# Optimization experiments

Measured on AMD Instinct MI355X. Metric: run time of the kernel, lower is better.

Reference implementation:

```python
import jax, jax.numpy as jnp
import numpy as np

B, T, F, UNITS = 64, 512, 128, 512
EPS = 1e-3  # Keras LayerNormalization default epsilon


def _layer_norm(x, g, b):
    m = x.mean(-1, keepdims=True)
    v = x.var(-1, keepdims=True)
    return (x - m) * jax.lax.rsqrt(v + EPS) * g + b


def _lstm(x, W, U, b):
    # Keras LSTM, gate order [i, f, c, o], zero initial state, tanh activations.
    Bsz = x.shape[0]
    Un = U.shape[0]
    h0 = jnp.zeros((Bsz, Un), x.dtype)
    c0 = jnp.zeros((Bsz, Un), x.dtype)
    xW = x @ W + b  # precompute input projection: [B, T, 4U]

    def step(carry, xw_t):
        h, c = carry
        z = xw_t + h @ U
        i, f, g, o = jnp.split(z, 4, axis=-1)
        c = jax.nn.sigmoid(f) * c + jax.nn.sigmoid(i) * jnp.tanh(g)
        h = jax.nn.sigmoid(o) * jnp.tanh(c)
        return (h, c), h

    (h, c), hs = jax.lax.scan(step, (h0, c0), jnp.swapaxes(xW, 0, 1))
    return jnp.swapaxes(hs, 0, 1), h, c  # seq out [B,T,U], final h, c


def _block(x, l0, l1, Wt, bt):
    block_in = x
    # layer 0: LSTM -> LayerNorm
    W, U, b, g, be = l0
    h, _, _ = _lstm(x, W, U, b)
    out = _layer_norm(h, g, be)
    # layer 1: LSTM -> LayerNorm -> Highway (units match layer 0)
    W, U, b, g, be = l1
    h, _, _ = _lstm(out, W, U, b)
    Hx = _layer_norm(h, g, be)
    Tx = jax.nn.sigmoid(out @ Wt + bt)  # transform gate, bias init -1.5
    hw = Hx * Tx + (1.0 - Tx) * out
    # quasi-dense: concat block input with last layer output
    return jnp.concatenate([block_in, hw], axis=-1)


def setup_inputs() -> dict:
    key = jax.random.key(0)
    ks = iter(jax.random.split(key, 32))
    def nrm(shape, scale):
        return jax.random.normal(next(ks), shape, jnp.float32) * scale
    d = {"x": jax.random.normal(next(ks), (B, T, F), jnp.float32)}
    in_dims = {"00": F, "01": UNITS, "10": F + UNITS, "11": UNITS}
    for tag, ind in in_dims.items():
        d[f"W{tag}"] = nrm((ind, 4 * UNITS), 1.0 / np.sqrt(ind))
        d[f"U{tag}"] = nrm((UNITS, 4 * UNITS), 1.0 / np.sqrt(UNITS))
        d[f"b{tag}"] = jnp.zeros((4 * UNITS,), jnp.float32)
        d[f"g{tag}"] = jnp.ones((UNITS,), jnp.float32)
        d[f"be{tag}"] = jnp.zeros((UNITS,), jnp.float32)
    for blk in ("0", "1"):
        d[f"Wt{blk}"] = nrm((UNITS, UNITS), 1.0 / np.sqrt(UNITS))
        d[f"bt{blk}"] = jnp.full((UNITS,), -1.5, jnp.float32)
    return d


def reference(x,
              W00, U00, b00, g00, be00,
              W01, U01, b01, g01, be01,
              Wt0, bt0,
              W10, U10, b10, g10, be10,
              W11, U11, b11, g11, be11,
              Wt1, bt1):
    out0 = _block(x, (W00, U00, b00, g00, be00), (W01, U01, b01, g01, be01), Wt0, bt0)
    out1 = _block(out0, (W10, U10, b10, g10, be10), (W11, U11, b11, g11, be11), Wt1, bt1)
    return out1  # [B, T, F + 2*UNITS]
```

## Files before the change

### kernel.cpp

```cpp
#include <hip/hip_runtime.h>
#include <hip/hip_bf16.h>

typedef unsigned short u16;
typedef unsigned int u32;
typedef __attribute__((ext_vector_type(8))) short short8;
typedef __attribute__((ext_vector_type(4))) short short4v;
typedef __attribute__((ext_vector_type(4))) float float4v;

#define Bsz 64
#define Tsz 512
#define Fsz 128
#define Usz 512
#define Gsz 2048
#define Msz 32768
#define OUTW 1152
#define BINW 640
#define NWG 16

__device__ __forceinline__ u16 f2b(float f) {
  u32 u = __float_as_uint(f);
  u32 r = (u + 0x7fffu + ((u >> 16) & 1u)) >> 16;
  return (u16)r;
}
__device__ __forceinline__ float b2f(u16 h) {
  return __uint_as_float(((u32)h) << 16);
}
__device__ __forceinline__ float sigm(float x) { return 1.f / (1.f + __expf(-x)); }
__device__ __forceinline__ float tanhfast(float x) { return 2.f / (1.f + __expf(-2.f * x)) - 1.f; }

__global__ void k_wt(const float* __restrict__ src, u16* __restrict__ dst, int K, int N) {
  __shared__ float t[32][33];
  int k0 = blockIdx.y << 5, n0 = blockIdx.x << 5;
  int tid = threadIdx.x;
  int r = tid >> 3, c = (tid & 7) << 2;
  float4v v = *(const float4v*)(src + (size_t)(k0 + r) * N + n0 + c);
  t[r][c + 0] = v[0]; t[r][c + 1] = v[1]; t[r][c + 2] = v[2]; t[r][c + 3] = v[3];
  __syncthreads();
  short4v o;
  o[0] = (short)f2b(t[c + 0][r]);
  o[1] = (short)f2b(t[c + 1][r]);
  o[2] = (short)f2b(t[c + 2][r]);
  o[3] = (short)f2b(t[c + 3][r]);
  *(short4v*)(dst + (size_t)(n0 + r) * K + k0 + c) = o;
}

__global__ void k_cvx(const float* __restrict__ x, float* __restrict__ dout, u16* __restrict__ bin) {
  int id = blockIdx.x * 256 + threadIdx.x;
  int row = id >> 5, c = (id & 31) << 2;
  float4v v = *(const float4v*)(x + (size_t)row * Fsz + c);
  *(float4v*)(dout + (size_t)row * OUTW + c) = v;
  short4v o;
  o[0] = (short)f2b(v[0]); o[1] = (short)f2b(v[1]);
  o[2] = (short)f2b(v[2]); o[3] = (short)f2b(v[3]);
  *(short4v*)(bin + (size_t)row * BINW + c) = o;
}

template <int PERM>
__launch_bounds__(256)
__global__ void k_gemm(const u16* __restrict__ A, int lda,
                       const u16* __restrict__ Bt, int K, int N,
                       const float* __restrict__ bias,
                       u16* __restrict__ C) {
  __shared__ u16 Al[128][40];
  __shared__ u16 Bl[64][40];
  int tid = threadIdx.x;
  int lane = tid & 63, wid = tid >> 6;
  int n0 = blockIdx.x << 6;
  size_t m0 = (size_t)blockIdx.y << 7;
  int mr = lane & 15, ko = (lane >> 4) << 3;
  float4v acc[2][4];
#pragma unroll
  for (int i = 0; i < 2; ++i)
#pragma unroll
    for (int j = 0; j < 4; ++j) acc[i][j] = (float4v){0.f, 0.f, 0.f, 0.f};

  for (int k0 = 0; k0 < K; k0 += 32) {
#pragma unroll
    for (int i = 0; i < 2; ++i) {
      int id = tid + (i << 8);
      int row = id >> 2, kc = (id & 3) << 3;
      int mlog = (int)m0 + row;
      size_t rp = PERM ? ((size_t)(mlog & 63) << 9) + (mlog >> 6) : (size_t)mlog;
      *(short8*)&Al[row][kc] = *(const short8*)(A + rp * (size_t)lda + k0 + kc);
    }
    {
      int row = tid >> 2, kc = (tid & 3) << 3;
      *(short8*)&Bl[row][kc] = *(const short8*)(Bt + (size_t)(n0 + row) * K + k0 + kc);
    }
    __syncthreads();
    short8 af0 = *(short8*)&Al[(wid << 5) + mr][ko];
    short8 af1 = *(short8*)&Al[(wid << 5) + 16 + mr][ko];
    short8 bf0 = *(short8*)&Bl[mr][ko];
    short8 bf1 = *(short8*)&Bl[16 + mr][ko];
    short8 bf2 = *(short8*)&Bl[32 + mr][ko];
    short8 bf3 = *(short8*)&Bl[48 + mr][ko];
    acc[0][0] = __builtin_amdgcn_mfma_f32_16x16x32_bf16(af0, bf0, acc[0][0], 0, 0, 0);
    acc[0][1] = __builtin_amdgcn_mfma_f32_16x16x32_bf16(af0, bf1, acc[0][1], 0, 0, 0);
    acc[0][2] = __builtin_amdgcn_mfma_f32_16x16x32_bf16(af0, bf2, acc[0][2], 0, 0, 0);
    acc[0][3] = __builtin_amdgcn_mfma_f32_16x16x32_bf16(af0, bf3, acc[0][3], 0, 0, 0);
    acc[1][0] = __builtin_amdgcn_mfma_f32_16x16x32_bf16(af1, bf0, acc[1][0], 0, 0, 0);
    acc[1][1] = __builtin_amdgcn_mfma_f32_16x16x32_bf16(af1, bf1, acc[1][1], 0, 0, 0);
    acc[1][2] = __builtin_amdgcn_mfma_f32_16x16x32_bf16(af1, bf2, acc[1][2], 0, 0, 0);
    acc[1][3] = __builtin_amdgcn_mfma_f32_16x16x32_bf16(af1, bf3, acc[1][3], 0, 0, 0);
    __syncthreads();
  }
  int rbase = (lane >> 4) << 2;
#pragma unroll
  for (int mt = 0; mt < 2; ++mt)
#pragma unroll
    for (int nt = 0; nt < 4; ++nt) {
      int n = n0 + (nt << 4) + mr;
      float bv = bias[n];
#pragma unroll
      for (int r = 0; r < 4; ++r) {
        int mlog = (int)m0 + (wid << 5) + (mt << 4) + rbase + r;
        float val = acc[mt][nt][r] + bv;
        if (PERM) {
          int b = mlog & 63, tt = mlog >> 6;
          int u = n & 511, g = n >> 9;
          C[(((size_t)tt * 512 + u) * 4 + g) * 64 + b] = f2b(val);
        } else {
          C[(size_t)mlog * N + n] = f2b(val);
        }
      }
    }
}

__global__ void k_zero(u32* __restrict__ p, int n32) {
  int id = blockIdx.x * 256 + threadIdx.x;
  for (int i = id; i < n32; i += gridDim.x * 256) p[i] = 0u;
}

__launch_bounds__(256, 1)
__global__ void k_scan(const u16* __restrict__ xw2,
                       const u16* __restrict__ Ut,
                       u16* __restrict__ hn,
                       u16* __restrict__ hseq,
                       u32* __restrict__ bar) {
  __shared__ u16 hl[32768];
  int tid = threadIdx.x;
  int lane = tid & 63, wid = tid >> 6;
  int mr = lane & 15, cg = lane >> 4;
  int ko = cg << 3;
  int gate = mr & 3, du = mr >> 2;
  int u0 = (blockIdx.x << 5) + (wid << 3);

  short8 af[2][16];
#pragma unroll
  for (int mt = 0; mt < 2; ++mt) {
    size_t urow = (size_t)(gate * Usz + u0 + (mt << 2) + du) * Usz;
#pragma unroll
    for (int kk = 0; kk < 16; ++kk)
      af[mt][kk] = *(const short8*)(Ut + urow + (kk << 5) + ko);
  }

  float cst[2][4];
#pragma unroll
  for (int mt = 0; mt < 2; ++mt)
#pragma unroll
    for (int nt = 0; nt < 4; ++nt) cst[mt][nt] = 0.f;

  u16 xwv[2][4][4], xwn[2][4][4];
#pragma unroll
  for (int mt = 0; mt < 2; ++mt) {
    int u = u0 + (mt << 2) + cg;
#pragma unroll
    for (int g = 0; g < 4; ++g)
#pragma unroll
      for (int nt = 0; nt < 4; ++nt)
        xwv[mt][g][nt] = xw2[(((size_t)0 * 512 + u) * 4 + g) * 64 + (nt << 4) + mr];
  }

  for (int t = 0; t < Tsz; ++t) {
    const u16* hsrc = hn + ((t & 1) ? 32768 : 0);
    u16* hdst = hn + ((t & 1) ? 0 : 32768);

    {
      const char* src = (const char*)hsrc;
#pragma unroll
      for (int j = 0; j < 16; ++j) {
        int b = (wid << 4) + j;
        int soff = ((lane << 4) ^ ((b & 7) << 4));
        __builtin_amdgcn_global_load_lds(
            (const __attribute__((address_space(1))) void*)(src + (size_t)b * 1024 + soff),
            (__attribute__((address_space(3))) void*)((char*)hl + (b << 10)),
            16, 0, 0);
      }
    }

    if (t + 1 < Tsz) {
#pragma unroll
      for (int mt = 0; mt < 2; ++mt) {
        int u = u0 + (mt << 2) + cg;
#pragma unroll
        for (int g = 0; g < 4; ++g)
#pragma unroll
          for (int nt = 0; nt < 4; ++nt)
            xwn[mt][g][nt] = xw2[(((size_t)(t + 1) * 512 + u) * 4 + g) * 64 + (nt << 4) + mr];
      }
    }

    float4v acc[2][4];
#pragma unroll
    for (int mt = 0; mt < 2; ++mt)
#pragma unroll
      for (int nt = 0; nt < 4; ++nt)
        acc[mt][nt] = (float4v){b2f(xwv[mt][0][nt]), b2f(xwv[mt][1][nt]),
                                b2f(xwv[mt][2][nt]), b2f(xwv[mt][3][nt])};

    __syncthreads();

#pragma unroll
    for (int kk = 0; kk < 16; ++kk) {
      short8 bfr[4];
#pragma unroll
      for (int nt = 0; nt < 4; ++nt) {
        int b = (nt << 4) + mr;
        int addr = (b << 10) + ((((kk << 6) + (cg << 4)) ^ ((b & 7) << 4)));
        bfr[nt] = *(const short8*)((const char*)hl + addr);
      }
#pragma unroll
      for (int mt = 0; mt < 2; ++mt)
#pragma unroll
        for (int nt = 0; nt < 4; ++nt)
          acc[mt][nt] = __builtin_amdgcn_mfma_f32_16x16x32_bf16(af[mt][kk], bfr[nt], acc[mt][nt], 0, 0, 0);
    }

#pragma unroll
    for (int mt = 0; mt < 2; ++mt)
#pragma unroll
      for (int nt = 0; nt < 4; ++nt) {
        float zi = acc[mt][nt][0], zf = acc[mt][nt][1];
        float zg = acc[mt][nt][2], zo = acc[mt][nt][3];
        float c = sigm(zf) * cst[mt][nt] + sigm(zi) * tanhfast(zg);
        cst[mt][nt] = c;
        float h = sigm(zo) * tanhfast(c);
        u16 hb = f2b(h);
        int b = (nt << 4) + mr;
        int u = u0 + (mt << 2) + cg;
        hdst[(size_t)b * Usz + u] = hb;
        hseq[((size_t)b * Tsz + t) * Usz + u] = hb;
      }

    if (t + 1 < Tsz) {
#pragma unroll
      for (int mt = 0; mt < 2; ++mt)
#pragma unroll
        for (int g = 0; g < 4; ++g)
#pragma unroll
          for (int nt = 0; nt < 4; ++nt) xwv[mt][g][nt] = xwn[mt][g][nt];
    }

    __syncthreads();
    if (tid == 0) {
      __threadfence();
      __hip_atomic_fetch_add(bar, 1u, __ATOMIC_RELEASE, __HIP_MEMORY_SCOPE_AGENT);
      u32 target = (u32)NWG * (u32)(t + 1);
      while (__hip_atomic_load(bar, __ATOMIC_ACQUIRE, __HIP_MEMORY_SCOPE_AGENT) < target)
        __builtin_amdgcn_s_sleep(1);
      __threadfence();
    }
    __syncthreads();
  }
}

__launch_bounds__(256)
__global__ void k_ln(const u16* __restrict__ in, const float* __restrict__ g,
                     const float* __restrict__ be, u16* __restrict__ out) {
  int lane = threadIdx.x & 63, wid = threadIdx.x >> 6;
  size_t row = (size_t)blockIdx.x * 4 + wid;
  short8 v = *(const short8*)(in + row * Usz + (lane << 3));
  float f[8];
  float s = 0.f, q = 0.f;
#pragma unroll
  for (int j = 0; j < 8; ++j) { f[j] = b2f((u16)v[j]); s += f[j]; q += f[j] * f[j]; }
#pragma unroll
  for (int o = 32; o > 0; o >>= 1) { s += __shfl_xor(s, o); q += __shfl_xor(q, o); }
  float mean = s * (1.f / 512.f);
  float var = q * (1.f / 512.f) - mean * mean;
  float rs = rsqrtf(var + 1e-3f);
  float4v g0 = *(const float4v*)(g + (lane << 3));
  float4v g1 = *(const float4v*)(g + (lane << 3) + 4);
  float4v e0 = *(const float4v*)(be + (lane << 3));
  float4v e1 = *(const float4v*)(be + (lane << 3) + 4);
  short8 o8;
#pragma unroll
  for (int j = 0; j < 8; ++j) {
    float gg = (j < 4) ? g0[j] : g1[j - 4];
    float ee = (j < 4) ? e0[j] : e1[j - 4];
    o8[j] = (short)f2b((f[j] - mean) * rs * gg + ee);
  }
  *(short8*)(out + row * Usz + (lane << 3)) = o8;
}

__launch_bounds__(256)
__global__ void k_lnhw(const u16* __restrict__ hs, const float* __restrict__ g,
                       const float* __restrict__ be, const u16* __restrict__ txr,
                       const u16* __restrict__ ob, float* __restrict__ dout,
                       int dcol, u16* __restrict__ bin) {
  int lane = threadIdx.x & 63, wid = threadIdx.x >> 6;
  size_t row = (size_t)blockIdx.x * 4 + wid;
  short8 v = *(const short8*)(hs + row * Usz + (lane << 3));
  float f[8];
  float s = 0.f, q = 0.f;
#pragma unroll
  for (int j = 0; j < 8; ++j) { f[j] = b2f((u16)v[j]); s += f[j]; q += f[j] * f[j]; }
#pragma unroll
  for (int o = 32; o > 0; o >>= 1) { s += __shfl_xor(s, o); q += __shfl_xor(q, o); }
  float mean = s * (1.f / 512.f);
  float var = q * (1.f / 512.f) - mean * mean;
  float rs = rsqrtf(var + 1e-3f);
  float4v g0 = *(const float4v*)(g + (lane << 3));
  float4v g1 = *(const float4v*)(g + (lane << 3) + 4);
  float4v e0 = *(const float4v*)(be + (lane << 3));
  float4v e1 = *(const float4v*)(be + (lane << 3) + 4);
  short8 tv = *(const short8*)(txr + row * Usz + (lane << 3));
  short8 ov = *(const short8*)(ob + row * Usz + (lane << 3));
  float hwv[8];
#pragma unroll
  for (int j = 0; j < 8; ++j) {
    float gg = (j < 4) ? g0[j] : g1[j - 4];
    float ee = (j < 4) ? e0[j] : e1[j - 4];
    float hx = (f[j] - mean) * rs * gg + ee;
    float tx = sigm(b2f((u16)tv[j]));
    float o_ = b2f((u16)ov[j]);
    hwv[j] = hx * tx + (1.f - tx) * o_;
  }
  float4v w0 = {hwv[0], hwv[1], hwv[2], hwv[3]};
  float4v w1 = {hwv[4], hwv[5], hwv[6], hwv[7]};
  *(float4v*)(dout + row * OUTW + dcol + (lane << 3)) = w0;
  *(float4v*)(dout + row * OUTW + dcol + (lane << 3) + 4) = w1;
  if (bin) {
    short8 hb;
#pragma unroll
    for (int j = 0; j < 8; ++j) hb[j] = (short)f2b(hwv[j]);
    *(short8*)(bin + row * BINW + 128 + (lane << 3)) = hb;
  }
}

extern "C" void kernel_launch(void* const* d_in, const int* in_sizes, int n_in,
                              void* d_out, int out_size, void* d_ws, size_t ws_size,
                              hipStream_t stream) {
  (void)in_sizes; (void)n_in; (void)out_size; (void)ws_size;
  const float* x = (const float*)d_in[0];
  const float* W[4]  = {(const float*)d_in[1],  (const float*)d_in[6],
                        (const float*)d_in[11], (const float*)d_in[16]};
  const float* U[4]  = {(const float*)d_in[2],  (const float*)d_in[7],
                        (const float*)d_in[12], (const float*)d_in[17]};
  const float* bb_[4] = {(const float*)d_in[3],  (const float*)d_in[8],
                        (const float*)d_in[13], (const float*)d_in[18]};
  const float* gg_[4] = {(const float*)d_in[4],  (const float*)d_in[9],
                        (const float*)d_in[14], (const float*)d_in[19]};
  const float* be_[4] = {(const float*)d_in[5],  (const float*)d_in[10],
                        (const float*)d_in[15], (const float*)d_in[20]};
  const float* Wtr[2] = {(const float*)d_in[21], (const float*)d_in[23]};
  const float* btr[2] = {(const float*)d_in[22], (const float*)d_in[24]};

  char* ws = (char*)d_ws;
  size_t off = 0;
  u16* xwb  = (u16*)(ws + off); off += (size_t)Msz * Gsz * 2;
  u16* hseq = (u16*)(ws + off); off += (size_t)Msz * Usz * 2;
  u16* mid  = (u16*)(ws + off); off += (size_t)Msz * Usz * 2;
  u16* bin  = (u16*)(ws + off); off += (size_t)Msz * BINW * 2;
  const int KIN[4] = {128, 512, 640, 512};
  u16* Wtb[4];
  for (int i = 0; i < 4; ++i) { Wtb[i] = (u16*)(ws + off); off += (size_t)Gsz * KIN[i] * 2; }
  u16* Utb[4];
  for (int i = 0; i < 4; ++i) { Utb[i] = (u16*)(ws + off); off += (size_t)Gsz * Usz * 2; }
  u16* Wtrb[2];
  for (int i = 0; i < 2; ++i) { Wtrb[i] = (u16*)(ws + off); off += (size_t)Usz * Usz * 2; }
  u16* hn = (u16*)(ws + off); off += 2 * (size_t)Bsz * Usz * 2;
  u32* bar = (u32*)(ws + off); off += 256;
  float* dout = (float*)d_out;

  for (int i = 0; i < 4; ++i)
    k_wt<<<dim3(Gsz / 32, KIN[i] / 32), 256, 0, stream>>>(W[i], Wtb[i], KIN[i], Gsz);
  for (int i = 0; i < 4; ++i)
    k_wt<<<dim3(Gsz / 32, Usz / 32), 256, 0, stream>>>(U[i], Utb[i], Usz, Gsz);
  for (int i = 0; i < 2; ++i)
    k_wt<<<dim3(Usz / 32, Usz / 32), 256, 0, stream>>>(Wtr[i], Wtrb[i], Usz, Usz);

  k_cvx<<<(Msz * 32) / 256, 256, 0, stream>>>(x, dout, bin);

  for (int blk = 0; blk < 2; ++blk) {
    int l0 = blk * 2, l1 = blk * 2 + 1;
    k_gemm<1><<<dim3(Gsz / 64, Msz / 128), 256, 0, stream>>>(bin, BINW, Wtb[l0], KIN[l0], Gsz, bb_[l0], xwb);
    k_zero<<<32, 256, 0, stream>>>((u32*)hn, 32768 + 64);
    k_scan<<<NWG, 256, 0, stream>>>(xwb, Utb[l0], hn, hseq, bar);
    k_ln<<<Msz / 4, 256, 0, stream>>>(hseq, gg_[l0], be_[l0], mid);
    k_gemm<1><<<dim3(Gsz / 64, Msz / 128), 256, 0, stream>>>(mid, Usz, Wtb[l1], Usz, Gsz, bb_[l1], xwb);
    k_zero<<<32, 256, 0, stream>>>((u32*)hn, 32768 + 64);
    k_scan<<<NWG, 256, 0, stream>>>(xwb, Utb[l1], hn, hseq, bar);
    k_gemm<0><<<dim3(Usz / 64, Msz / 128), 256, 0, stream>>>(mid, Usz, Wtrb[blk], Usz, Usz, btr[blk], xwb);
    k_lnhw<<<Msz / 4, 256, 0, stream>>>(hseq, gg_[l1], be_[l1], xwb, mid, dout,
                                        blk == 0 ? 128 : 640, blk == 0 ? bin : (u16*)nullptr);
  }
}
```

Before: 13.09 ms.

## Replace atomic counter barrier with per-WG flags and read h from hseq directly

The scan kernel drops the double-buffered h scratch and reads the previous step's hidden state straight from a time-major hseq buffer. A single atomic counter barrier is replaced by per-workgroup padded flags polled by one wavefront. It also adds coalesced LDS-staged h writes, gate-interleaved xW loads as short4 vectors, and launches 128 blocks of which only every eighth works, presumably to spread the active workgroups across XCDs. Downstream the LN/GEMM stages are re-permuted to consume time-major hseq, which risks layout bugs but cuts barrier contention and scattered stores.

```diff
diff --git a/kernel.cpp b/kernel.cpp
--- a/kernel.cpp
+++ b/kernel.cpp
@@ -6,6 +6,8 @@
 typedef __attribute__((ext_vector_type(8))) short short8;
 typedef __attribute__((ext_vector_type(4))) short short4v;
 typedef __attribute__((ext_vector_type(4))) float float4v;
+typedef __attribute__((ext_vector_type(2))) unsigned int uint2v;
+typedef __attribute__((ext_vector_type(4))) unsigned int uint4v;
 
 #define Bsz 64
 #define Tsz 512
@@ -16,6 +18,7 @@
 #define OUTW 1152
 #define BINW 640
 #define NWG 16
+#define FLSTR 32
 
 __device__ __forceinline__ u16 f2b(float f) {
   u32 u = __float_as_uint(f);
@@ -55,7 +58,7 @@
   *(short4v*)(bin + (size_t)row * BINW + c) = o;
 }
 
-template <int PERM>
+template <int APERM, int CPERM>
 __launch_bounds__(256)
 __global__ void k_gemm(const u16* __restrict__ A, int lda,
                        const u16* __restrict__ Bt, int K, int N,
@@ -80,7 +83,7 @@
       int id = tid + (i << 8);
       int row = id >> 2, kc = (id & 3) << 3;
       int mlog = (int)m0 + row;
-      size_t rp = PERM ? ((size_t)(mlog & 63) << 9) + (mlog >> 6) : (size_t)mlog;
+      size_t rp = APERM ? ((size_t)(mlog & 63) << 9) + (mlog >> 6) : (size_t)mlog;
       *(short8*)&Al[row][kc] = *(const short8*)(A + rp * (size_t)lda + k0 + kc);
     }
     {
@@ -115,10 +118,10 @@
       for (int r = 0; r < 4; ++r) {
         int mlog = (int)m0 + (wid << 5) + (mt << 4) + rbase + r;
         float val = acc[mt][nt][r] + bv;
-        if (PERM) {
+        if (CPERM) {
           int b = mlog & 63, tt = mlog >> 6;
           int u = n & 511, g = n >> 9;
-          C[(((size_t)tt * 512 + u) * 4 + g) * 64 + b] = f2b(val);
+          C[((((size_t)tt * 512 + u) * 64 + b) << 2) + g] = f2b(val);
         } else {
           C[(size_t)mlog * N + n] = f2b(val);
         }
@@ -134,16 +137,17 @@
 __launch_bounds__(256, 1)
 __global__ void k_scan(const u16* __restrict__ xw2,
                        const u16* __restrict__ Ut,
-                       u16* __restrict__ hn,
                        u16* __restrict__ hseq,
                        u32* __restrict__ bar) {
+  if (blockIdx.x & 7) return;
+  int wg = blockIdx.x >> 3;
   __shared__ u16 hl[32768];
+  u16* hout = hl;
   int tid = threadIdx.x;
   int lane = tid & 63, wid = tid >> 6;
   int mr = lane & 15, cg = lane >> 4;
-  int ko = cg << 3;
   int gate = mr & 3, du = mr >> 2;
-  int u0 = (blockIdx.x << 5) + (wid << 3);
+  int u0 = (wg << 5) + (wid << 3);
 
   short8 af[2][16];
 #pragma unroll
@@ -151,7 +155,7 @@
     size_t urow = (size_t)(gate * Usz + u0 + (mt << 2) + du) * Usz;
 #pragma unroll
     for (int kk = 0; kk < 16; ++kk)
-      af[mt][kk] = *(const short8*)(Ut + urow + (kk << 5) + ko);
+      af[mt][kk] = *(const short8*)(Ut + urow + (kk << 5) + (cg << 3));
   }
 
   float cst[2][4];
@@ -160,72 +164,75 @@
 #pragma unroll
     for (int nt = 0; nt < 4; ++nt) cst[mt][nt] = 0.f;
 
-  u16 xwv[2][4][4], xwn[2][4][4];
-#pragma unroll
-  for (int mt = 0; mt < 2; ++mt) {
-    int u = u0 + (mt << 2) + cg;
-#pragma unroll
-    for (int g = 0; g < 4; ++g)
+  short4v xwc[2][4], xwn[2][4];
+#pragma unroll
+  for (int mt = 0; mt < 2; ++mt)
+#pragma unroll
+    for (int nt = 0; nt < 4; ++nt)
+      xwc[mt][nt] = *(const short4v*)(xw2 + ((((size_t)0 * 512 + u0 + (mt << 2) + cg) * 64
+                                             + (nt << 4) + mr) << 2));
+
+  for (int t = 0; t < Tsz; ++t) {
+    float4v acc[2][4];
+#pragma unroll
+    for (int mt = 0; mt < 2; ++mt)
 #pragma unroll
       for (int nt = 0; nt < 4; ++nt)
-        xwv[mt][g][nt] = xw2[(((size_t)0 * 512 + u) * 4 + g) * 64 + (nt << 4) + mr];
-  }
-
-  for (int t = 0; t < Tsz; ++t) {
-    const u16* hsrc = hn + ((t & 1) ? 32768 : 0);
-    u16* hdst = hn + ((t & 1) ? 0 : 32768);
-
-    {
-      const char* src = (const char*)hsrc;
-#pragma unroll
-      for (int j = 0; j < 16; ++j) {
-        int b = (wid << 4) + j;
-        int soff = ((lane << 4) ^ ((b & 7) << 4));
-        __builtin_amdgcn_global_load_lds(
-            (const __attribute__((address_space(1))) void*)(src + (size_t)b * 1024 + soff),
-            (__attribute__((address_space(3))) void*)((char*)hl + (b << 10)),
-            16, 0, 0);
-      }
-    }
+        acc[mt][nt] = (float4v){b2f((u16)xwc[mt][nt][0]), b2f((u16)xwc[mt][nt][1]),
+                                b2f((u16)xwc[mt][nt][2]), b2f((u16)xwc[mt][nt][3])};
 
     if (t + 1 < Tsz) {
 #pragma unroll
-      for (int mt = 0; mt < 2; ++mt) {
-        int u = u0 + (mt << 2) + cg;
-#pragma unroll
-        for (int g = 0; g < 4; ++g)
+      for (int mt = 0; mt < 2; ++mt)
+#pragma unroll
+        for (int nt = 0; nt < 4; ++nt)
+          xwn[mt][nt] = *(const short4v*)(xw2 + ((((size_t)(t + 1) * 512 + u0 + (mt << 2) + cg) * 64
+                                                 + (nt << 4) + mr) << 2));
+    }
+
+    if (t > 0) {
+      if (wid == 0) {
+        u32 tgt = (u32)t;
+        for (;;) {
+          u32 v = (lane < NWG)
+                    ? __hip_atomic_load(bar + lane * FLSTR, __ATOMIC_RELAXED, __HIP_MEMORY_SCOPE_AGENT)
+                    : 0xFFFFFFFFu;
+          if (__all(v >= tgt)) break;
+          __builtin_amdgcn_s_sleep(1);
+        }
+        __threadfence();
+      }
+      __syncthreads();
+
+      {
+        const char* hsrc = (const char*)hseq + ((size_t)(t - 1) << 16);
+#pragma unroll
+        for (int j = 0; j < 16; ++j) {
+          int c = (wid << 4) + j;
+          const char* src = hsrc + ((((c & 3) << 4) + mr) << 10) + ((c >> 2) << 6) + (cg << 4);
+          __builtin_amdgcn_global_load_lds(
+              (const __attribute__((address_space(1))) void*)src,
+              (__attribute__((address_space(3))) void*)(hl + (c << 9)),
+              16, 0, 0);
+        }
+      }
+      __syncthreads();
+
+#pragma unroll
+      for (int kk = 0; kk < 16; ++kk) {
+        short8 bfr[4];
+#pragma unroll
+        for (int nt = 0; nt < 4; ++nt)
+          bfr[nt] = *(const short8*)(hl + ((((kk << 2) + nt) << 9) + (lane << 3)));
+#pragma unroll
+        for (int mt = 0; mt < 2; ++mt)
 #pragma unroll
           for (int nt = 0; nt < 4; ++nt)
-            xwn[mt][g][nt] = xw2[(((size_t)(t + 1) * 512 + u) * 4 + g) * 64 + (nt << 4) + mr];
-      }
-    }
-
-    float4v acc[2][4];
-#pragma unroll
-    for (int mt = 0; mt < 2; ++mt)
-#pragma unroll
-      for (int nt = 0; nt < 4; ++nt)
-        acc[mt][nt] = (float4v){b2f(xwv[mt][0][nt]), b2f(xwv[mt][1][nt]),
-                                b2f(xwv[mt][2][nt]), b2f(xwv[mt][3][nt])};
-
-    __syncthreads();
-
-#pragma unroll
-    for (int kk = 0; kk < 16; ++kk) {
-      short8 bfr[4];
-#pragma unroll
-      for (int nt = 0; nt < 4; ++nt) {
-        int b = (nt << 4) + mr;
-        int addr = (b << 10) + ((((kk << 6) + (cg << 4)) ^ ((b & 7) << 4)));
-        bfr[nt] = *(const short8*)((const char*)hl + addr);
-      }
-#pragma unroll
-      for (int mt = 0; mt < 2; ++mt)
-#pragma unroll
-        for (int nt = 0; nt < 4; ++nt)
-          acc[mt][nt] = __builtin_amdgcn_mfma_f32_16x16x32_bf16(af[mt][kk], bfr[nt], acc[mt][nt], 0, 0, 0);
-    }
-
+            acc[mt][nt] = __builtin_amdgcn_mfma_f32_16x16x32_bf16(af[mt][kk], bfr[nt], acc[mt][nt], 0, 0, 0);
+      }
+    }
+
+    u16 hb[2][4];
 #pragma unroll
     for (int mt = 0; mt < 2; ++mt)
 #pragma unroll
@@ -234,33 +241,43 @@
         float zg = acc[mt][nt][2], zo = acc[mt][nt][3];
         float c = sigm(zf) * cst[mt][nt] + sigm(zi) * tanhfast(zg);
         cst[mt][nt] = c;
-        float h = sigm(zo) * tanhfast(c);
-        u16 hb = f2b(h);
+        hb[mt][nt] = f2b(sigm(zo) * tanhfast(c));
+      }
+
+    __syncthreads();
+
+#pragma unroll
+    for (int mt = 0; mt < 2; ++mt)
+#pragma unroll
+      for (int nt = 0; nt < 4; ++nt) {
         int b = (nt << 4) + mr;
-        int u = u0 + (mt << 2) + cg;
-        hdst[(size_t)b * Usz + u] = hb;
-        hseq[((size_t)b * Tsz + t) * Usz + u] = hb;
-      }
-
-    if (t + 1 < Tsz) {
-#pragma unroll
-      for (int mt = 0; mt < 2; ++mt)
-#pragma unroll
-        for (int g = 0; g < 4; ++g)
-#pragma unroll
-          for (int nt = 0; nt < 4; ++nt) xwv[mt][g][nt] = xwn[mt][g][nt];
-    }
-
+        int ul = (wid << 3) + (mt << 2) + cg;
+        *(u16*)((char*)hout + (b << 6) + (((ul << 1)) ^ ((b & 7) << 3))) = hb[mt][nt];
+      }
     __syncthreads();
+
+    {
+      int b = tid >> 2, q = tid & 3, s = (b & 7) << 3;
+      const char* hrow = (const char*)hout + (b << 6);
+      uint2v A0 = *(const uint2v*)(hrow + (((q << 4) | 0) ^ s));
+      uint2v A1 = *(const uint2v*)(hrow + (((q << 4) | 8) ^ s));
+      uint4v val; val[0] = A0[0]; val[1] = A0[1]; val[2] = A1[0]; val[3] = A1[1];
+      char* dst = (char*)hseq + ((size_t)t << 16) + (b << 10) + (wg << 6) + (q << 4);
+      *(uint4v*)dst = val;
+    }
+    __syncthreads();
+
     if (tid == 0) {
       __threadfence();
-      __hip_atomic_fetch_add(bar, 1u, __ATOMIC_RELEASE, __HIP_MEMORY_SCOPE_AGENT);
-      u32 target = (u32)NWG * (u32)(t + 1);
-      while (__hip_atomic_load(bar, __ATOMIC_ACQUIRE, __HIP_MEMORY_SCOPE_AGENT) < target)
-        __builtin_amdgcn_s_sleep(1);
-      __threadfence();
-    }
-    __syncthreads();
+      __hip_atomic_store(bar + wg * FLSTR, (u32)(t + 1), __ATOMIC_RELEASE, __HIP_MEMORY_SCOPE_AGENT);
+    }
+
+    if (t + 1 < Tsz) {
+#pragma unroll
+      for (int mt = 0; mt < 2; ++mt)
+#pragma unroll
+        for (int nt = 0; nt < 4; ++nt) xwc[mt][nt] = xwn[mt][nt];
+    }
   }
 }
 
@@ -326,15 +343,16 @@
     float o_ = b2f((u16)ov[j]);
     hwv[j] = hx * tx + (1.f - tx) * o_;
   }
+  size_t orow = ((row & 63) << 9) + (row >> 6);
   float4v w0 = {hwv[0], hwv[1], hwv[2], hwv[3]};
   float4v w1 = {hwv[4], hwv[5], hwv[6], hwv[7]};
-  *(float4v*)(dout + row * OUTW + dcol + (lane << 3)) = w0;
-  *(float4v*)(dout + row * OUTW + dcol + (lane << 3) + 4) = w1;
+  *(float4v*)(dout + orow * OUTW + dcol + (lane << 3)) = w0;
+  *(float4v*)(dout + orow * OUTW + dcol + (lane << 3) + 4) = w1;
   if (bin) {
     short8 hb;
 #pragma unroll
     for (int j = 0; j < 8; ++j) hb[j] = (short)f2b(hwv[j]);
-    *(short8*)(bin + row * BINW + 128 + (lane << 3)) = hb;
+    *(short8*)(bin + orow * BINW + 128 + (lane << 3)) = hb;
   }
 }
 
@@ -369,8 +387,7 @@
   for (int i = 0; i < 4; ++i) { Utb[i] = (u16*)(ws + off); off += (size_t)Gsz * Usz * 2; }
   u16* Wtrb[2];
   for (int i = 0; i < 2; ++i) { Wtrb[i] = (u16*)(ws + off); off += (size_t)Usz * Usz * 2; }
-  u16* hn = (u16*)(ws + off); off += 2 * (size_t)Bsz * Usz * 2;
-  u32* bar = (u32*)(ws + off); off += 256;
+  u32* bar = (u32*)(ws + off); off += 4096;
   float* dout = (float*)d_out;
 
   for (int i = 0; i < 4; ++i)
@@ -384,14 +401,14 @@
 
   for (int blk = 0; blk < 2; ++blk) {
     int l0 = blk * 2, l1 = blk * 2 + 1;
-    k_gemm<1><<<dim3(Gsz / 64, Msz / 128), 256, 0, stream>>>(bin, BINW, Wtb[l0], KIN[l0], Gsz, bb_[l0], xwb);
-    k_zero<<<32, 256, 0, stream>>>((u32*)hn, 32768 + 64);
-    k_scan<<<NWG, 256, 0, stream>>>(xwb, Utb[l0], hn, hseq, bar);
+    k_gemm<1, 1><<<dim3(Gsz / 64, Msz / 128), 256, 0, stream>>>(bin, BINW, Wtb[l0], KIN[l0], Gsz, bb_[l0], xwb);
+    k_zero<<<1, 256, 0, stream>>>(bar, NWG * FLSTR);
+    k_scan<<<128, 256, 0, stream>>>(xwb, Utb[l0], hseq, bar);
     k_ln<<<Msz / 4, 256, 0, stream>>>(hseq, gg_[l0], be_[l0], mid);
-    k_gemm<1><<<dim3(Gsz / 64, Msz / 128), 256, 0, stream>>>(mid, Usz, Wtb[l1], Usz, Gsz, bb_[l1], xwb);
-    k_zero<<<32, 256, 0, stream>>>((u32*)hn, 32768 + 64);
-    k_scan<<<NWG, 256, 0, stream>>>(xwb, Utb[l1], hn, hseq, bar);
-    k_gemm<0><<<dim3(Usz / 64, Msz / 128), 256, 0, stream>>>(mid, Usz, Wtrb[blk], Usz, Usz, btr[blk], xwb);
+    k_gemm<0, 1><<<dim3(Gsz / 64, Msz / 128), 256, 0, stream>>>(mid, Usz, Wtb[l1], Usz, Gsz, bb_[l1], xwb);
+    k_zero<<<1, 256, 0, stream>>>(bar, NWG * FLSTR);
+    k_scan<<<128, 256, 0, stream>>>(xwb, Utb[l1], hseq, bar);
+    k_gemm<0, 0><<<dim3(Usz / 64, Msz / 128), 256, 0, stream>>>(mid, Usz, Wtrb[blk], Usz, Usz, btr[blk], xwb);
     k_lnhw<<<Msz / 4, 256, 0, stream>>>(hseq, gg_[l1], be_[l1], xwb, mid, dout,
                                         blk == 0 ? 128 : 640, blk == 0 ? bin : (u16*)nullptr);
   }
```

New measurement: 28.31 ms. 2.16x slower.
